# Performance work log

Hardware: AMD Instinct MI355X
Metric: run time of the kernel (lower is better)

Reference implementation:

```python
import jax, jax.numpy as jnp
import numpy as np

H = 2048      # hidden_size
I = 768       # moe_intermediate_size
E = 32        # num_experts
K = 4         # num_experts_per_tok
B, S = 1, 2048


def setup_inputs() -> dict:
    key = jax.random.key(0)
    k0, k1, k2, k3, k4 = jax.random.split(key, 5)
    return {
        "hidden_states": jax.random.normal(k0, (B, S, H), dtype=jnp.float32),
        "gate_w": jax.random.normal(k1, (E, H), dtype=jnp.float32) * 0.02,
        "Wg": jax.random.normal(k2, (E, H, I), dtype=jnp.float32) * 0.02,
        "Wu": jax.random.normal(k3, (E, H, I), dtype=jnp.float32) * 0.02,
        "Wd": jax.random.normal(k4, (E, I, H), dtype=jnp.float32) * 0.02,
        "top_k": K,
    }


def reference(hidden_states, gate_w, Wg, Wu, Wd, top_k):
    b, s, h = hidden_states.shape
    x = hidden_states.reshape(-1, h)                      # [T, H]
    T = x.shape[0]
    e = gate_w.shape[0]

    # Router: softmax over experts, then top-k and renormalize (norm_topk_prob=True)
    logits = x @ gate_w.T                                 # [T, E]
    probs = jax.nn.softmax(logits, axis=-1)
    w, sel = jax.lax.top_k(probs, top_k)                  # [T, K]
    w = w / jnp.sum(w, axis=-1, keepdims=True)

    # Scatter top-k weights into a dense [T, E] combine matrix
    combine = jnp.zeros((T, e), dtype=x.dtype).at[
        jnp.arange(T)[:, None], sel].add(w)               # [T, E]

    # Expert SiLU-gated MLPs, computed densely for all experts (mirrors the
    # ttnn path that repeats tokens across local experts and masks on combine)
    g = jnp.einsum('th,ehi->eti', x, Wg)                  # [E, T, I]
    u = jnp.einsum('th,ehi->eti', x, Wu)                  # [E, T, I]
    a = jax.nn.silu(g) * u                                # [E, T, I]
    # Fold combine weights in before the down projection to avoid an [E,T,H] temp
    a = a * combine.T[:, :, None]                         # [E, T, I]
    out = jnp.einsum('eti,eih->th', a, Wd)                # [T, H]
    return out.reshape(b, s, h)
```

## Files before the change

### kernel.cpp

```cpp
#include <hip/hip_runtime.h>
#include <cstdint>
#include <cstddef>

#define TDIM 2048
#define HDIM 2048
#define IDIM 768
#define EXP  32
#define TOPK 4
#define TKTOT 8192
#define MAXMETA 96
#define CHUNK 256
#define NMETA 64

typedef __attribute__((ext_vector_type(8))) short short8;
typedef __attribute__((ext_vector_type(4))) float f32x4;

constexpr size_t OFF_XBF = 0;
constexpr size_t OFF_ACT = OFF_XBF + (size_t)TDIM * HDIM * 2;
constexpr size_t OFF_LOG = OFF_ACT + (size_t)TKTOT * IDIM * 2;
constexpr size_t OFF_SEL = OFF_LOG + (size_t)TDIM * EXP * 4;
constexpr size_t OFF_WTS = OFF_SEL + (size_t)TDIM * TOPK * 4;
constexpr size_t OFF_STK = OFF_WTS + (size_t)TDIM * TOPK * 4;
constexpr size_t OFF_SW  = OFF_STK + (size_t)TKTOT * 4;
constexpr size_t OFF_INV = OFF_SW  + (size_t)TKTOT * 4;
constexpr size_t OFF_CNT = OFF_INV + (size_t)TDIM * TOPK * 4;
constexpr size_t OFF_CUR = OFF_CNT + EXP * 4;
constexpr size_t OFF_OFS = OFF_CUR + EXP * 4;
constexpr size_t OFF_MET = OFF_OFS + (EXP + 1) * 4;
constexpr size_t OFF_NB  = OFF_MET + MAXMETA * 2 * 4;
constexpr size_t OFF_TMP = (OFF_NB + 4 + 255) & ~(size_t)255;
constexpr size_t TMP_BYTES = (size_t)TKTOT * HDIM * 4;

__device__ __forceinline__ unsigned short f2bf(float f) {
  unsigned u = __float_as_uint(f);
  u = (u + 0x7fffu + ((u >> 16) & 1u)) >> 16;
  return (unsigned short)u;
}
__device__ __forceinline__ unsigned pk2(float a, float b) {
  return (unsigned)f2bf(a) | ((unsigned)f2bf(b) << 16);
}
__device__ __forceinline__ void async16(void* lds, const void* g) {
  __builtin_amdgcn_global_load_lds((const __attribute__((address_space(1))) void*)g,
                                   (__attribute__((address_space(3))) void*)lds, 16, 0, 0);
}

__global__ __launch_bounds__(256) void k_cvt(const float* __restrict__ x,
                                             unsigned short* __restrict__ xb) {
  int i = blockIdx.x * 256 + threadIdx.x;
  const float4* s = (const float4*)x;
  float4 a = s[2 * i], b = s[2 * i + 1];
  uint4 o;
  o.x = pk2(a.x, a.y); o.y = pk2(a.z, a.w);
  o.z = pk2(b.x, b.y); o.w = pk2(b.z, b.w);
  ((uint4*)xb)[i] = o;
}

__global__ __launch_bounds__(256) void k_router(const float* __restrict__ x,
                                                const float* __restrict__ gw,
                                                float* __restrict__ logits) {
  __shared__ float smx[4 * HDIM];
  int tid = threadIdx.x;
  int t0 = blockIdx.x * 4;
  const float4* src = (const float4*)(x + (size_t)t0 * HDIM);
  float4* dst = (float4*)smx;
#pragma unroll
  for (int i = 0; i < 8; i++) dst[i * 256 + tid] = src[i * 256 + tid];
  __syncthreads();
  int e = tid >> 3, sl = tid & 7;
  float acc[4] = {0.f, 0.f, 0.f, 0.f};
  const float* gptr = gw + (size_t)e * HDIM + sl * 256;
#pragma unroll 4
  for (int j = 0; j < 64; j++) {
    float4 g4 = *(const float4*)(gptr + j * 4);
#pragma unroll
    for (int tt = 0; tt < 4; tt++) {
      float4 xa = *(const float4*)&smx[tt * HDIM + sl * 256 + j * 4];
      acc[tt] += g4.x * xa.x + g4.y * xa.y + g4.z * xa.z + g4.w * xa.w;
    }
  }
  __syncthreads();
#pragma unroll
  for (int tt = 0; tt < 4; tt++) smx[(tt * EXP + e) * 8 + sl] = acc[tt];
  __syncthreads();
  if (tid < 128) {
    int tt = tid >> 5, ee = tid & 31;
    float s = 0.f;
#pragma unroll
    for (int q = 0; q < 8; q++) s += smx[(tt * EXP + ee) * 8 + q];
    logits[(size_t)(t0 + tt) * EXP + ee] = s;
  }
}

__global__ __launch_bounds__(256) void k_topk(const float* __restrict__ logits,
                                              int* __restrict__ sel,
                                              float* __restrict__ wts,
                                              int* __restrict__ cnt) {
  int t = blockIdx.x * 256 + threadIdx.x;
  float p[EXP];
  float mx = -1e30f;
#pragma unroll
  for (int e = 0; e < EXP; e++) { p[e] = logits[(size_t)t * EXP + e]; mx = fmaxf(mx, p[e]); }
#pragma unroll
  for (int e = 0; e < EXP; e++) p[e] = __expf(p[e] - mx);
  unsigned used = 0; int si[TOPK]; float sv[TOPK]; float tot = 0.f;
  for (int k = 0; k < TOPK; k++) {
    float bm = -1.f; int bi = 0;
#pragma unroll
    for (int e = 0; e < EXP; e++) {
      bool ok = !((used >> e) & 1) && (p[e] > bm);
      bm = ok ? p[e] : bm;
      bi = ok ? e : bi;
    }
    used |= 1u << bi; si[k] = bi; sv[k] = bm; tot += bm;
  }
  float inv = 1.f / tot;
#pragma unroll
  for (int k = 0; k < TOPK; k++) {
    sel[t * TOPK + k] = si[k];
    wts[t * TOPK + k] = sv[k] * inv;
    atomicAdd(&cnt[si[k]], 1);
  }
}

__global__ void k_scan(const int* __restrict__ cnt, int* __restrict__ offs,
                       int* __restrict__ cur, int* __restrict__ meta,
                       int* __restrict__ nb) {
  if (threadIdx.x == 0 && blockIdx.x == 0) {
    int off = 0, n = 0;
    for (int e = 0; e < EXP; e++) {
      offs[e] = off; cur[e] = off;
      int c = cnt[e];
      for (int r = 0; r < c && n < NMETA; r += CHUNK) { meta[n * 2] = e; meta[n * 2 + 1] = r; n++; }
      off += c;
    }
    offs[EXP] = off;
    nb[0] = n;
  }
}

__global__ __launch_bounds__(256) void k_scatter(const int* __restrict__ sel,
                                                 const float* __restrict__ wts,
                                                 int* __restrict__ cur,
                                                 int* __restrict__ stok,
                                                 float* __restrict__ sw,
                                                 int* __restrict__ inv) {
  int t = blockIdx.x * 256 + threadIdx.x;
#pragma unroll
  for (int k = 0; k < TOPK; k++) {
    int e = sel[t * TOPK + k];
    int p = atomicAdd(&cur[e], 1);
    stok[p] = t;
    sw[p] = wts[t * TOPK + k];
    inv[t * TOPK + k] = p;
  }
}

__global__ __launch_bounds__(512, 1) void k_gemm1n(
    const float* __restrict__ Wg, const float* __restrict__ Wu,
    const unsigned short* __restrict__ xb,
    const int* __restrict__ stok, const float* __restrict__ sw,
    const int* __restrict__ cnt, const int* __restrict__ offs,
    const int* __restrict__ meta, const int* __restrict__ nb,
    unsigned short* __restrict__ act) {
  int bid = (blockIdx.x & 7) * 8 + (blockIdx.x >> 3);
  if (bid >= nb[0]) return;
  int e = meta[bid * 2], r0 = meta[bid * 2 + 1];
  int pos0 = offs[e] + r0;
  int rows = min(CHUNK, cnt[e] - r0);
  int n0 = blockIdx.y * 64;

  __shared__ unsigned short smA[2][CHUNK * 64];
  __shared__ unsigned short smBg[2][64 * 64];
  __shared__ unsigned short smBu[2][64 * 64];
  __shared__ int smTok[CHUNK];
  __shared__ float smW[CHUNK];

  int tid = threadIdx.x;
  if (tid < CHUNK) {
    int rr = (tid < rows) ? tid : 0;
    smTok[tid] = stok[pos0 + rr];
    smW[tid] = (tid < rows) ? sw[pos0 + tid] : 0.f;
  }
  __syncthreads();

  int lane = tid & 63, w = tid >> 6;
  int waveM = w >> 1, waveN = w & 1;

  const unsigned short* aC[4];
#pragma unroll
  for (int p = 0; p < 4; p++) {
    int r = p * 64 + w * 8 + (lane >> 3);
    aC[p] = xb + (size_t)smTok[r] * HDIM + (((lane & 7) ^ (r & 7)) << 3);
  }
  size_t wb = (size_t)e * HDIM * IDIM;
  int bn = tid & 63, kh = tid >> 6;
  const float* pG = Wg + wb + (size_t)(kh * 8) * IDIM + n0 + bn;
  const float* pU = Wu + wb + (size_t)(kh * 8) * IDIM + n0 + bn;
  int bOff = bn * 64 + ((kh ^ (bn & 7)) << 3);

  f32x4 accG[4][2], accU[4][2];
#pragma unroll
  for (int a = 0; a < 4; a++)
#pragma unroll
    for (int b = 0; b < 2; b++) { accG[a][b] = {0.f,0.f,0.f,0.f}; accU[a][b] = {0.f,0.f,0.f,0.f}; }

  int lm = lane & 15, lq = lane >> 4;
  float vg[8], vu[8];

#pragma unroll
  for (int p = 0; p < 4; p++) async16(&smA[0][(p * 64 + w * 8) * 64], aC[p]);
#pragma unroll
  for (int j = 0; j < 8; j++) { vg[j] = pG[(size_t)j * IDIM]; vu[j] = pU[(size_t)j * IDIM]; }
  {
    short8 og, ou;
#pragma unroll
    for (int z = 0; z < 8; z++) { og[z] = (short)f2bf(vg[z]); ou[z] = (short)f2bf(vu[z]); }
    *(short8*)&smBg[0][bOff] = og;
    *(short8*)&smBu[0][bOff] = ou;
  }
  __syncthreads();

  const int NK = HDIM / 64;
  for (int kt = 0; kt < NK; kt++) {
    int c = kt & 1;
    if (kt + 1 < NK) {
#pragma unroll
      for (int p = 0; p < 4; p++) { aC[p] += 64; async16(&smA[c ^ 1][(p * 64 + w * 8) * 64], aC[p]); }
      pG += (size_t)64 * IDIM; pU += (size_t)64 * IDIM;
#pragma unroll
      for (int j = 0; j < 8; j++) { vg[j] = pG[(size_t)j * IDIM]; vu[j] = pU[(size_t)j * IDIM]; }
    }
#pragma unroll
    for (int s = 0; s < 2; s++) {
      int kq = s * 4 + lq;
      short8 af[4], bg[2], bu[2];
#pragma unroll
      for (int mt = 0; mt < 4; mt++) {
        int m = waveM * 64 + mt * 16 + lm;
        af[mt] = *(const short8*)&smA[c][m * 64 + ((kq ^ (m & 7)) << 3)];
      }
#pragma unroll
      for (int nt = 0; nt < 2; nt++) {
        int n = waveN * 32 + nt * 16 + lm;
        int off = n * 64 + ((kq ^ (n & 7)) << 3);
        bg[nt] = *(const short8*)&smBg[c][off];
        bu[nt] = *(const short8*)&smBu[c][off];
      }
#pragma unroll
      for (int mt = 0; mt < 4; mt++)
#pragma unroll
        for (int nt = 0; nt < 2; nt++) {
          accG[mt][nt] = __builtin_amdgcn_mfma_f32_16x16x32_bf16(af[mt], bg[nt], accG[mt][nt], 0, 0, 0);
          accU[mt][nt] = __builtin_amdgcn_mfma_f32_16x16x32_bf16(af[mt], bu[nt], accU[mt][nt], 0, 0, 0);
        }
    }
    if (kt + 1 < NK) {
      short8 og, ou;
#pragma unroll
      for (int z = 0; z < 8; z++) { og[z] = (short)f2bf(vg[z]); ou[z] = (short)f2bf(vu[z]); }
      *(short8*)&smBg[c ^ 1][bOff] = og;
      *(short8*)&smBu[c ^ 1][bOff] = ou;
    }
    __syncthreads();
  }

#pragma unroll
  for (int mt = 0; mt < 4; mt++)
#pragma unroll
    for (int nt = 0; nt < 2; nt++) {
      int n = n0 + waveN * 32 + nt * 16 + lm;
#pragma unroll
      for (int i = 0; i < 4; i++) {
        int r = waveM * 64 + mt * 16 + lq * 4 + i;
        if (r < rows) {
          float g = accG[mt][nt][i], u = accU[mt][nt][i];
          float sg = g / (1.f + __expf(-g));
          act[(size_t)(pos0 + r) * IDIM + n] = f2bf(sg * u * smW[r]);
        }
      }
    }
}

__global__ __launch_bounds__(512, 1) void k_gemm2n(
    const float* __restrict__ Wd, const unsigned short* __restrict__ act,
    const int* __restrict__ stok, const int* __restrict__ cnt,
    const int* __restrict__ offs, const int* __restrict__ meta,
    const int* __restrict__ nb, float* __restrict__ dst, int mode) {
  int bid = (blockIdx.x & 7) * 8 + (blockIdx.x >> 3);
  if (bid >= nb[0]) return;
  int e = meta[bid * 2], r0 = meta[bid * 2 + 1];
  int pos0 = offs[e] + r0;
  int rows = min(CHUNK, cnt[e] - r0);
  int n0 = blockIdx.y * 128;

  __shared__ unsigned short smA[2][CHUNK * 64];
  __shared__ unsigned short smB[2][128 * 64];
  __shared__ int smTok[CHUNK];

  int tid = threadIdx.x;
  if (tid < CHUNK) {
    int rr = (tid < rows) ? tid : 0;
    smTok[tid] = stok[pos0 + rr];
  }
  __syncthreads();

  int lane = tid & 63, w = tid >> 6;
  int waveM = w >> 1, waveN = w & 1;

  const unsigned short* aC[4];
#pragma unroll
  for (int p = 0; p < 4; p++) {
    int r = p * 64 + w * 8 + (lane >> 3);
    int pp = pos0 + r; if (pp > TKTOT - 1) pp = TKTOT - 1;
    aC[p] = act + (size_t)pp * IDIM + (((lane & 7) ^ (r & 7)) << 3);
  }
  size_t wb = (size_t)e * IDIM * HDIM;
  int bn = tid & 127, kh = tid >> 7;
  const float* pD = Wd + wb + (size_t)(kh * 16) * HDIM + n0 + bn;

  f32x4 acc[4][4];
#pragma unroll
  for (int a = 0; a < 4; a++)
#pragma unroll
    for (int b = 0; b < 4; b++) acc[a][b] = {0.f, 0.f, 0.f, 0.f};

  int lm = lane & 15, lq = lane >> 4;
  float v[16];

#pragma unroll
  for (int p = 0; p < 4; p++) async16(&smA[0][(p * 64 + w * 8) * 64], aC[p]);
#pragma unroll
  for (int j = 0; j < 16; j++) v[j] = pD[(size_t)j * HDIM];
#pragma unroll
  for (int jj = 0; jj < 2; jj++) {
    short8 o;
#pragma unroll
    for (int z = 0; z < 8; z++) o[z] = (short)f2bf(v[jj * 8 + z]);
    *(short8*)&smB[0][bn * 64 + (((kh * 2 + jj) ^ (bn & 7)) << 3)] = o;
  }
  __syncthreads();

  const int NK = IDIM / 64;
  for (int kt = 0; kt < NK; kt++) {
    int c = kt & 1;
    if (kt + 1 < NK) {
#pragma unroll
      for (int p = 0; p < 4; p++) { aC[p] += 64; async16(&smA[c ^ 1][(p * 64 + w * 8) * 64], aC[p]); }
      pD += (size_t)64 * HDIM;
#pragma unroll
      for (int j = 0; j < 16; j++) v[j] = pD[(size_t)j * HDIM];
    }
#pragma unroll
    for (int s = 0; s < 2; s++) {
      int kq = s * 4 + lq;
      short8 af[4], bf[4];
#pragma unroll
      for (int mt = 0; mt < 4; mt++) {
        int m = waveM * 64 + mt * 16 + lm;
        af[mt] = *(const short8*)&smA[c][m * 64 + ((kq ^ (m & 7)) << 3)];
      }
#pragma unroll
      for (int nt = 0; nt < 4; nt++) {
        int n = waveN * 64 + nt * 16 + lm;
        bf[nt] = *(const short8*)&smB[c][n * 64 + ((kq ^ (n & 7)) << 3)];
      }
#pragma unroll
      for (int mt = 0; mt < 4; mt++)
#pragma unroll
        for (int nt = 0; nt < 4; nt++)
          acc[mt][nt] = __builtin_amdgcn_mfma_f32_16x16x32_bf16(af[mt], bf[nt], acc[mt][nt], 0, 0, 0);
    }
    if (kt + 1 < NK) {
#pragma unroll
      for (int jj = 0; jj < 2; jj++) {
        short8 o;
#pragma unroll
        for (int z = 0; z < 8; z++) o[z] = (short)f2bf(v[jj * 8 + z]);
        *(short8*)&smB[c ^ 1][bn * 64 + (((kh * 2 + jj) ^ (bn & 7)) << 3)] = o;
      }
    }
    __syncthreads();
  }

#pragma unroll
  for (int mt = 0; mt < 4; mt++)
#pragma unroll
    for (int nt = 0; nt < 4; nt++) {
      int n = n0 + waveN * 64 + nt * 16 + lm;
#pragma unroll
      for (int i = 0; i < 4; i++) {
        int r = waveM * 64 + mt * 16 + lq * 4 + i;
        if (r < rows) {
          float val = acc[mt][nt][i];
          if (mode == 0) {
            dst[(size_t)(pos0 + r) * HDIM + n] = val;
          } else {
            __hip_atomic_fetch_add(&dst[(size_t)smTok[r] * HDIM + n], val,
                                   __ATOMIC_RELAXED, __HIP_MEMORY_SCOPE_AGENT);
          }
        }
      }
    }
}

__global__ __launch_bounds__(256) void k_reduce(const float* __restrict__ tmp,
                                                const int* __restrict__ inv,
                                                float* __restrict__ out) {
  int u = blockIdx.x * 256 + threadIdx.x;
  int t = u >> 9, c = u & 511;
  int i0 = inv[t * 4 + 0], i1 = inv[t * 4 + 1], i2 = inv[t * 4 + 2], i3 = inv[t * 4 + 3];
  float4 a = *(const float4*)(tmp + (size_t)i0 * HDIM + c * 4);
  float4 b = *(const float4*)(tmp + (size_t)i1 * HDIM + c * 4);
  float4 d = *(const float4*)(tmp + (size_t)i2 * HDIM + c * 4);
  float4 e = *(const float4*)(tmp + (size_t)i3 * HDIM + c * 4);
  float4 s;
  s.x = a.x + b.x + d.x + e.x;
  s.y = a.y + b.y + d.y + e.y;
  s.z = a.z + b.z + d.z + e.z;
  s.w = a.w + b.w + d.w + e.w;
  *(float4*)(out + (size_t)t * HDIM + c * 4) = s;
}

extern "C" void kernel_launch(void* const* d_in, const int* in_sizes, int n_in,
                              void* d_out, int out_size, void* d_ws, size_t ws_size,
                              hipStream_t stream) {
  const float* x  = (const float*)d_in[0];
  const float* gw = (const float*)d_in[1];
  const float* Wg = (const float*)d_in[2];
  const float* Wu = (const float*)d_in[3];
  const float* Wd = (const float*)d_in[4];
  float* out = (float*)d_out;

  char* ws = (char*)d_ws;
  unsigned short* xb  = (unsigned short*)(ws + OFF_XBF);
  unsigned short* act = (unsigned short*)(ws + OFF_ACT);
  float* logits = (float*)(ws + OFF_LOG);
  int*   sel    = (int*)(ws + OFF_SEL);
  float* wts    = (float*)(ws + OFF_WTS);
  int*   stok   = (int*)(ws + OFF_STK);
  float* sw     = (float*)(ws + OFF_SW);
  int*   inv    = (int*)(ws + OFF_INV);
  int*   cnt    = (int*)(ws + OFF_CNT);
  int*   cur    = (int*)(ws + OFF_CUR);
  int*   offs   = (int*)(ws + OFF_OFS);
  int*   meta   = (int*)(ws + OFF_MET);
  int*   nb     = (int*)(ws + OFF_NB);
  float* tmp    = (float*)(ws + OFF_TMP);

  bool useTmp = ws_size >= OFF_TMP + TMP_BYTES;

  hipMemsetAsync(cnt, 0, EXP * 4, stream);
  k_cvt<<<(TDIM * HDIM / 8) / 256, 256, 0, stream>>>(x, xb);
  k_router<<<TDIM / 4, 256, 0, stream>>>(x, gw, logits);
  k_topk<<<TDIM / 256, 256, 0, stream>>>(logits, sel, wts, cnt);
  k_scan<<<1, 64, 0, stream>>>(cnt, offs, cur, meta, nb);
  k_scatter<<<TDIM / 256, 256, 0, stream>>>(sel, wts, cur, stok, sw, inv);

  k_gemm1n<<<dim3(NMETA, IDIM / 64), 512, 0, stream>>>(Wg, Wu, xb, stok, sw, cnt, offs, meta, nb, act);
  if (useTmp) {
    k_gemm2n<<<dim3(NMETA, HDIM / 128), 512, 0, stream>>>(Wd, act, stok, cnt, offs, meta, nb, tmp, 0);
    k_reduce<<<(TDIM * 512) / 256, 256, 0, stream>>>(tmp, inv, out);
  } else {
    hipMemsetAsync(out, 0, (size_t)TDIM * HDIM * 4, stream);
    k_gemm2n<<<dim3(NMETA, HDIM / 128), 512, 0, stream>>>(Wd, act, stok, cnt, offs, meta, nb, out, 1);
  }
}
```

Before: 806.5 us.

## Split expert chunks into 128-row blocks and load A fragments directly from global

Each 256-row expert chunk is now split across two 256-thread blocks of 128 rows, with launch bounds set for three blocks per CU. The shared-memory A tile and its async global-to-LDS loads are removed, so each wave reads its MFMA A fragments straight from global memory (bf16 activations or gathered token rows), which relies on L2 for reuse. B tile staging is redistributed so each thread converts twice as many weight elements. The aim is more occupancy and less LDS, at the cost of more global or cache traffic for A and no prefetch overlap on those loads.

```diff
diff --git a/kernel.cpp b/kernel.cpp
--- a/kernel.cpp
+++ b/kernel.cpp
@@ -39,10 +39,6 @@
 __device__ __forceinline__ unsigned pk2(float a, float b) {
   return (unsigned)f2bf(a) | ((unsigned)f2bf(b) << 16);
 }
-__device__ __forceinline__ void async16(void* lds, const void* g) {
-  __builtin_amdgcn_global_load_lds((const __attribute__((address_space(1))) void*)g,
-                                   (__attribute__((address_space(3))) void*)lds, 16, 0, 0);
-}
 
 __global__ __launch_bounds__(256) void k_cvt(const float* __restrict__ x,
                                              unsigned short* __restrict__ xb) {
@@ -155,48 +151,46 @@
   }
 }
 
-__global__ __launch_bounds__(512, 1) void k_gemm1n(
+__global__ __launch_bounds__(256, 3) void k_gemm1n(
     const float* __restrict__ Wg, const float* __restrict__ Wu,
     const unsigned short* __restrict__ xb,
     const int* __restrict__ stok, const float* __restrict__ sw,
     const int* __restrict__ cnt, const int* __restrict__ offs,
     const int* __restrict__ meta, const int* __restrict__ nb,
     unsigned short* __restrict__ act) {
-  int bid = (blockIdx.x & 7) * 8 + (blockIdx.x >> 3);
-  if (bid >= nb[0]) return;
-  int e = meta[bid * 2], r0 = meta[bid * 2 + 1];
+  int raw = blockIdx.x;
+  int L = (raw & 7) * 16 + (raw >> 3);
+  int cidx = L >> 1, half = L & 1;
+  if (cidx >= nb[0]) return;
+  int e = meta[cidx * 2], r0 = meta[cidx * 2 + 1] + half * 128;
   int pos0 = offs[e] + r0;
-  int rows = min(CHUNK, cnt[e] - r0);
+  int rows = cnt[e] - r0;
+  if (rows <= 0) return;
+  if (rows > 128) rows = 128;
   int n0 = blockIdx.y * 64;
 
-  __shared__ unsigned short smA[2][CHUNK * 64];
   __shared__ unsigned short smBg[2][64 * 64];
   __shared__ unsigned short smBu[2][64 * 64];
-  __shared__ int smTok[CHUNK];
-  __shared__ float smW[CHUNK];
 
   int tid = threadIdx.x;
-  if (tid < CHUNK) {
-    int rr = (tid < rows) ? tid : 0;
-    smTok[tid] = stok[pos0 + rr];
-    smW[tid] = (tid < rows) ? sw[pos0 + tid] : 0.f;
-  }
-  __syncthreads();
-
   int lane = tid & 63, w = tid >> 6;
   int waveM = w >> 1, waveN = w & 1;
-
-  const unsigned short* aC[4];
-#pragma unroll
-  for (int p = 0; p < 4; p++) {
-    int r = p * 64 + w * 8 + (lane >> 3);
-    aC[p] = xb + (size_t)smTok[r] * HDIM + (((lane & 7) ^ (r & 7)) << 3);
-  }
+  int lm = lane & 15, lq = lane >> 4;
+
+  const unsigned short* aP[4];
+#pragma unroll
+  for (int mt = 0; mt < 4; mt++) {
+    int m = waveM * 64 + mt * 16 + lm;
+    int mc = (m < rows) ? m : 0;
+    aP[mt] = xb + (size_t)stok[pos0 + mc] * HDIM + lq * 8;
+  }
+
   size_t wb = (size_t)e * HDIM * IDIM;
-  int bn = tid & 63, kh = tid >> 6;
-  const float* pG = Wg + wb + (size_t)(kh * 8) * IDIM + n0 + bn;
-  const float* pU = Wu + wb + (size_t)(kh * 8) * IDIM + n0 + bn;
-  int bOff = bn * 64 + ((kh ^ (bn & 7)) << 3);
+  int bn = lane, kh = w;
+  const float* pG = Wg + wb + (size_t)(kh * 16) * IDIM + n0 + bn;
+  const float* pU = Wu + wb + (size_t)(kh * 16) * IDIM + n0 + bn;
+  int bO0 = bn * 64 + (((kh * 2 + 0) ^ (bn & 7)) << 3);
+  int bO1 = bn * 64 + (((kh * 2 + 1) ^ (bn & 7)) << 3);
 
   f32x4 accG[4][2], accU[4][2];
 #pragma unroll
@@ -204,41 +198,39 @@
 #pragma unroll
     for (int b = 0; b < 2; b++) { accG[a][b] = {0.f,0.f,0.f,0.f}; accU[a][b] = {0.f,0.f,0.f,0.f}; }
 
-  int lm = lane & 15, lq = lane >> 4;
-  float vg[8], vu[8];
-
-#pragma unroll
-  for (int p = 0; p < 4; p++) async16(&smA[0][(p * 64 + w * 8) * 64], aC[p]);
-#pragma unroll
-  for (int j = 0; j < 8; j++) { vg[j] = pG[(size_t)j * IDIM]; vu[j] = pU[(size_t)j * IDIM]; }
+  float vg[16], vu[16];
+#pragma unroll
+  for (int j = 0; j < 16; j++) { vg[j] = pG[(size_t)j * IDIM]; vu[j] = pU[(size_t)j * IDIM]; }
   {
-    short8 og, ou;
-#pragma unroll
-    for (int z = 0; z < 8; z++) { og[z] = (short)f2bf(vg[z]); ou[z] = (short)f2bf(vu[z]); }
-    *(short8*)&smBg[0][bOff] = og;
-    *(short8*)&smBu[0][bOff] = ou;
+    short8 og0, ou0, og1, ou1;
+#pragma unroll
+    for (int z = 0; z < 8; z++) {
+      og0[z] = (short)f2bf(vg[z]);     ou0[z] = (short)f2bf(vu[z]);
+      og1[z] = (short)f2bf(vg[8 + z]); ou1[z] = (short)f2bf(vu[8 + z]);
+    }
+    *(short8*)&smBg[0][bO0] = og0; *(short8*)&smBu[0][bO0] = ou0;
+    *(short8*)&smBg[0][bO1] = og1; *(short8*)&smBu[0][bO1] = ou1;
   }
   __syncthreads();
 
   const int NK = HDIM / 64;
   for (int kt = 0; kt < NK; kt++) {
     int c = kt & 1;
+    short8 af[8];
+#pragma unroll
+    for (int s = 0; s < 2; s++)
+#pragma unroll
+      for (int mt = 0; mt < 4; mt++)
+        af[s * 4 + mt] = *(const short8*)(aP[mt] + s * 32);
     if (kt + 1 < NK) {
-#pragma unroll
-      for (int p = 0; p < 4; p++) { aC[p] += 64; async16(&smA[c ^ 1][(p * 64 + w * 8) * 64], aC[p]); }
       pG += (size_t)64 * IDIM; pU += (size_t)64 * IDIM;
 #pragma unroll
-      for (int j = 0; j < 8; j++) { vg[j] = pG[(size_t)j * IDIM]; vu[j] = pU[(size_t)j * IDIM]; }
+      for (int j = 0; j < 16; j++) { vg[j] = pG[(size_t)j * IDIM]; vu[j] = pU[(size_t)j * IDIM]; }
     }
 #pragma unroll
     for (int s = 0; s < 2; s++) {
       int kq = s * 4 + lq;
-      short8 af[4], bg[2], bu[2];
-#pragma unroll
-      for (int mt = 0; mt < 4; mt++) {
-        int m = waveM * 64 + mt * 16 + lm;
-        af[mt] = *(const short8*)&smA[c][m * 64 + ((kq ^ (m & 7)) << 3)];
-      }
+      short8 bg[2], bu[2];
 #pragma unroll
       for (int nt = 0; nt < 2; nt++) {
         int n = waveN * 32 + nt * 16 + lm;
@@ -250,16 +242,21 @@
       for (int mt = 0; mt < 4; mt++)
 #pragma unroll
         for (int nt = 0; nt < 2; nt++) {
-          accG[mt][nt] = __builtin_amdgcn_mfma_f32_16x16x32_bf16(af[mt], bg[nt], accG[mt][nt], 0, 0, 0);
-          accU[mt][nt] = __builtin_amdgcn_mfma_f32_16x16x32_bf16(af[mt], bu[nt], accU[mt][nt], 0, 0, 0);
+          accG[mt][nt] = __builtin_amdgcn_mfma_f32_16x16x32_bf16(af[s * 4 + mt], bg[nt], accG[mt][nt], 0, 0, 0);
+          accU[mt][nt] = __builtin_amdgcn_mfma_f32_16x16x32_bf16(af[s * 4 + mt], bu[nt], accU[mt][nt], 0, 0, 0);
         }
     }
+#pragma unroll
+    for (int mt = 0; mt < 4; mt++) aP[mt] += 64;
     if (kt + 1 < NK) {
-      short8 og, ou;
-#pragma unroll
-      for (int z = 0; z < 8; z++) { og[z] = (short)f2bf(vg[z]); ou[z] = (short)f2bf(vu[z]); }
-      *(short8*)&smBg[c ^ 1][bOff] = og;
-      *(short8*)&smBu[c ^ 1][bOff] = ou;
+      short8 og0, ou0, og1, ou1;
+#pragma unroll
+      for (int z = 0; z < 8; z++) {
+        og0[z] = (short)f2bf(vg[z]);     ou0[z] = (short)f2bf(vu[z]);
+        og1[z] = (short)f2bf(vg[8 + z]); ou1[z] = (short)f2bf(vu[8 + z]);
+      }
+      *(short8*)&smBg[c ^ 1][bO0] = og0; *(short8*)&smBu[c ^ 1][bO0] = ou0;
+      *(short8*)&smBg[c ^ 1][bO1] = og1; *(short8*)&smBu[c ^ 1][bO1] = ou1;
     }
     __syncthreads();
   }
@@ -275,48 +272,51 @@
         if (r < rows) {
           float g = accG[mt][nt][i], u = accU[mt][nt][i];
           float sg = g / (1.f + __expf(-g));
-          act[(size_t)(pos0 + r) * IDIM + n] = f2bf(sg * u * smW[r]);
+          act[(size_t)(pos0 + r) * IDIM + n] = f2bf(sg * u * sw[pos0 + r]);
         }
       }
     }
 }
 
-__global__ __launch_bounds__(512, 1) void k_gemm2n(
+__global__ __launch_bounds__(256, 3) void k_gemm2n(
     const float* __restrict__ Wd, const unsigned short* __restrict__ act,
     const int* __restrict__ stok, const int* __restrict__ cnt,
     const int* __restrict__ offs, const int* __restrict__ meta,
     const int* __restrict__ nb, float* __restrict__ dst, int mode) {
-  int bid = (blockIdx.x & 7) * 8 + (blockIdx.x >> 3);
-  if (bid >= nb[0]) return;
-  int e = meta[bid * 2], r0 = meta[bid * 2 + 1];
+  int raw = blockIdx.x;
+  int L = (raw & 7) * 16 + (raw >> 3);
+  int cidx = L >> 1, half = L & 1;
+  if (cidx >= nb[0]) return;
+  int e = meta[cidx * 2], r0 = meta[cidx * 2 + 1] + half * 128;
   int pos0 = offs[e] + r0;
-  int rows = min(CHUNK, cnt[e] - r0);
+  int rows = cnt[e] - r0;
+  if (rows <= 0) return;
+  if (rows > 128) rows = 128;
   int n0 = blockIdx.y * 128;
 
-  __shared__ unsigned short smA[2][CHUNK * 64];
   __shared__ unsigned short smB[2][128 * 64];
-  __shared__ int smTok[CHUNK];
 
   int tid = threadIdx.x;
-  if (tid < CHUNK) {
-    int rr = (tid < rows) ? tid : 0;
-    smTok[tid] = stok[pos0 + rr];
-  }
-  __syncthreads();
-
   int lane = tid & 63, w = tid >> 6;
   int waveM = w >> 1, waveN = w & 1;
-
-  const unsigned short* aC[4];
-#pragma unroll
-  for (int p = 0; p < 4; p++) {
-    int r = p * 64 + w * 8 + (lane >> 3);
-    int pp = pos0 + r; if (pp > TKTOT - 1) pp = TKTOT - 1;
-    aC[p] = act + (size_t)pp * IDIM + (((lane & 7) ^ (r & 7)) << 3);
-  }
+  int lm = lane & 15, lq = lane >> 4;
+
+  const unsigned short* aP[4];
+#pragma unroll
+  for (int mt = 0; mt < 4; mt++) {
+    int m = waveM * 64 + mt * 16 + lm;
+    int mc = (m < rows) ? m : 0;
+    int pp = pos0 + mc; if (pp > TKTOT - 1) pp = TKTOT - 1;
+    aP[mt] = act + (size_t)pp * IDIM + lq * 8;
+  }
+
   size_t wb = (size_t)e * IDIM * HDIM;
   int bn = tid & 127, kh = tid >> 7;
-  const float* pD = Wd + wb + (size_t)(kh * 16) * HDIM + n0 + bn;
+  const float* pD = Wd + wb + (size_t)(kh * 32) * HDIM + n0 + bn;
+  int bO[4];
+#pragma unroll
+  for (int jj = 0; jj < 4; jj++)
+    bO[jj] = bn * 64 + (((kh * 4 + jj) ^ (bn & 7)) << 3);
 
   f32x4 acc[4][4];
 #pragma unroll
@@ -324,41 +324,36 @@
 #pragma unroll
     for (int b = 0; b < 4; b++) acc[a][b] = {0.f, 0.f, 0.f, 0.f};
 
-  int lm = lane & 15, lq = lane >> 4;
-  float v[16];
-
-#pragma unroll
-  for (int p = 0; p < 4; p++) async16(&smA[0][(p * 64 + w * 8) * 64], aC[p]);
-#pragma unroll
-  for (int j = 0; j < 16; j++) v[j] = pD[(size_t)j * HDIM];
-#pragma unroll
-  for (int jj = 0; jj < 2; jj++) {
+  float v[32];
+#pragma unroll
+  for (int j = 0; j < 32; j++) v[j] = pD[(size_t)j * HDIM];
+#pragma unroll
+  for (int jj = 0; jj < 4; jj++) {
     short8 o;
 #pragma unroll
     for (int z = 0; z < 8; z++) o[z] = (short)f2bf(v[jj * 8 + z]);
-    *(short8*)&smB[0][bn * 64 + (((kh * 2 + jj) ^ (bn & 7)) << 3)] = o;
+    *(short8*)&smB[0][bO[jj]] = o;
   }
   __syncthreads();
 
   const int NK = IDIM / 64;
   for (int kt = 0; kt < NK; kt++) {
     int c = kt & 1;
+    short8 af[8];
+#pragma unroll
+    for (int s = 0; s < 2; s++)
+#pragma unroll
+      for (int mt = 0; mt < 4; mt++)
+        af[s * 4 + mt] = *(const short8*)(aP[mt] + s * 32);
     if (kt + 1 < NK) {
-#pragma unroll
-      for (int p = 0; p < 4; p++) { aC[p] += 64; async16(&smA[c ^ 1][(p * 64 + w * 8) * 64], aC[p]); }
       pD += (size_t)64 * HDIM;
 #pragma unroll
-      for (int j = 0; j < 16; j++) v[j] = pD[(size_t)j * HDIM];
+      for (int j = 0; j < 32; j++) v[j] = pD[(size_t)j * HDIM];
     }
 #pragma unroll
     for (int s = 0; s < 2; s++) {
       int kq = s * 4 + lq;
-      short8 af[4], bf[4];
-#pragma unroll
-      for (int mt = 0; mt < 4; mt++) {
-        int m = waveM * 64 + mt * 16 + lm;
-        af[mt] = *(const short8*)&smA[c][m * 64 + ((kq ^ (m & 7)) << 3)];
-      }
+      short8 bf[4];
 #pragma unroll
       for (int nt = 0; nt < 4; nt++) {
         int n = waveN * 64 + nt * 16 + lm;
@@ -368,15 +363,17 @@
       for (int mt = 0; mt < 4; mt++)
 #pragma unroll
         for (int nt = 0; nt < 4; nt++)
-          acc[mt][nt] = __builtin_amdgcn_mfma_f32_16x16x32_bf16(af[mt], bf[nt], acc[mt][nt], 0, 0, 0);
-    }
+          acc[mt][nt] = __builtin_amdgcn_mfma_f32_16x16x32_bf16(af[s * 4 + mt], bf[nt], acc[mt][nt], 0, 0, 0);
+    }
+#pragma unroll
+    for (int mt = 0; mt < 4; mt++) aP[mt] += 64;
     if (kt + 1 < NK) {
 #pragma unroll
-      for (int jj = 0; jj < 2; jj++) {
+      for (int jj = 0; jj < 4; jj++) {
         short8 o;
 #pragma unroll
         for (int z = 0; z < 8; z++) o[z] = (short)f2bf(v[jj * 8 + z]);
-        *(short8*)&smB[c ^ 1][bn * 64 + (((kh * 2 + jj) ^ (bn & 7)) << 3)] = o;
+        *(short8*)&smB[c ^ 1][bO[jj]] = o;
       }
     }
     __syncthreads();
@@ -395,7 +392,7 @@
           if (mode == 0) {
             dst[(size_t)(pos0 + r) * HDIM + n] = val;
           } else {
-            __hip_atomic_fetch_add(&dst[(size_t)smTok[r] * HDIM + n], val,
+            __hip_atomic_fetch_add(&dst[(size_t)stok[pos0 + r] * HDIM + n], val,
                                    __ATOMIC_RELAXED, __HIP_MEMORY_SCOPE_AGENT);
           }
         }
@@ -456,12 +453,12 @@
   k_scan<<<1, 64, 0, stream>>>(cnt, offs, cur, meta, nb);
   k_scatter<<<TDIM / 256, 256, 0, stream>>>(sel, wts, cur, stok, sw, inv);
 
-  k_gemm1n<<<dim3(NMETA, IDIM / 64), 512, 0, stream>>>(Wg, Wu, xb, stok, sw, cnt, offs, meta, nb, act);
+  k_gemm1n<<<dim3(2 * NMETA, IDIM / 64), 256, 0, stream>>>(Wg, Wu, xb, stok, sw, cnt, offs, meta, nb, act);
   if (useTmp) {
-    k_gemm2n<<<dim3(NMETA, HDIM / 128), 512, 0, stream>>>(Wd, act, stok, cnt, offs, meta, nb, tmp, 0);
+    k_gemm2n<<<dim3(2 * NMETA, HDIM / 128), 256, 0, stream>>>(Wd, act, stok, cnt, offs, meta, nb, tmp, 0);
     k_reduce<<<(TDIM * 512) / 256, 256, 0, stream>>>(tmp, inv, out);
   } else {
     hipMemsetAsync(out, 0, (size_t)TDIM * HDIM * 4, stream);
-    k_gemm2n<<<dim3(NMETA, HDIM / 128), 512, 0, stream>>>(Wd, act, stok, cnt, offs, meta, nb, out, 1);
-  }
-}
+    k_gemm2n<<<dim3(2 * NMETA, HDIM / 128), 256, 0, stream>>>(Wd, act, stok, cnt, offs, meta, nb, out, 1);
+  }
+}
```

Measured after the change: 1.150 ms. 42.6% more time.
